# Kernel optimization log

Measured on AMD Instinct MI355X. Metric: run time of the kernel, lower is better.

The kernel has to match this reference:

```python
import jax, jax.numpy as jnp
import numpy as np

EPS = 1e-8

def setup_inputs() -> dict:
    key = jax.random.key(0)
    k1, k2 = jax.random.split(key)
    B, N, M, D = 8, 4096, 4096, 3
    x1 = jax.random.normal(k1, (B, N, D), dtype=jnp.float32)
    y1 = jax.random.normal(k2, (B, M, D), dtype=jnp.float32)
    return {"x1": x1, "y1": y1}

def reference(x1, y1):
    # Faithful to: dist = sqrt(1e-8 + sum((x1[:,None,:,:] - y1[:,:,None,:])**2, -1))
    # computed via the Gram-matrix expansion to avoid the (B,M,N,D) intermediate.
    x_sq = jnp.sum(x1 * x1, axis=-1)                 # (B, N)
    y_sq = jnp.sum(y1 * y1, axis=-1)                 # (B, M)
    xy = jnp.einsum('bmd,bnd->bmn', y1, x1)          # (B, M, N)
    d2 = jnp.maximum(y_sq[:, :, None] + x_sq[:, None, :] - 2.0 * xy, 0.0)
    dist = jnp.sqrt(EPS + d2)                        # (B, M, N)
    min1 = jnp.min(dist, axis=1)                     # (B, N): nearest y for each x
    min2 = jnp.min(dist, axis=2)                     # (B, M): nearest x for each y
    return jnp.mean(min1) + jnp.mean(min2)
```

## Files before the change

### kernel.cpp

```cpp
#include <hip/hip_runtime.h>

constexpr int B = 8;
constexpr int N = 4096;
constexpr int PTS = B * N;
constexpr int TOT = 2 * PTS;

#define TPB 256
#define R 4
#define CHUNK 128
#define NCHUNK (N / CHUNK)
#define NTILE (N / (TPB * R))

__global__ __launch_bounds__(256) void prep(
        const float* __restrict__ x1, const float* __restrict__ y1,
        float4* __restrict__ qpre, float* __restrict__ out) {
    int tid = blockIdx.x * 256 + threadIdx.x;
    if (tid == 0) out[0] = 0.0f;
    if (tid >= TOT) return;
    int dir = tid >> 15;
    int p   = tid & (PTS - 1);
    const float* src = dir ? x1 : y1;
    float qx = src[3 * p], qy = src[3 * p + 1], qz = src[3 * p + 2];
    float qq = fmaf(qx, qx, fmaf(qy, qy, qz * qz));
    qpre[tid] = make_float4(qx, qy, qz, qq);
}

__global__ __launch_bounds__(TPB) void chamfer_min3(
        const float* __restrict__ x1, const float* __restrict__ y1,
        const float4* __restrict__ qpre,
        float* __restrict__ partials) {
    __shared__ float4 qs[CHUNK];

    const int dir   = blockIdx.y / NCHUNK;
    const int chunk = blockIdx.y % NCHUNK;
    const int b     = blockIdx.z;
    const int tile  = blockIdx.x;

    const float4* qp = qpre + (size_t)dir * PTS + (size_t)b * N + chunk * CHUNK;
    if (threadIdx.x < CHUNK) qs[threadIdx.x] = qp[threadIdx.x];

    const float* own = dir ? y1 : x1;
    const int ibase = tile * (TPB * R) + threadIdx.x;
    float mx[R], my[R], mz[R], xx[R], acc[R];
    #pragma unroll
    for (int r = 0; r < R; r++) {
        const float* pp = own + ((size_t)b * N + ibase + r * TPB) * 3;
        float px = pp[0], py = pp[1], pz = pp[2];
        mx[r] = -2.0f * px; my[r] = -2.0f * py; mz[r] = -2.0f * pz;
        xx[r] = fmaf(px, px, fmaf(py, py, pz * pz));
        acc[r] = 3.4e38f;
    }

    __syncthreads();

    #pragma unroll 4
    for (int j = 0; j < CHUNK; j++) {
        float4 q = qs[j];
        #pragma unroll
        for (int r = 0; r < R; r++) {
            float g = fmaf(mx[r], q.x, fmaf(my[r], q.y, fmaf(mz[r], q.z, q.w)));
            acc[r] = fminf(acc[r], g);
        }
    }

    float* dst = partials + (size_t)chunk * TOT + (size_t)dir * PTS + (size_t)b * N;
    #pragma unroll
    for (int r = 0; r < R; r++) {
        dst[ibase + r * TPB] = fmaxf(acc[r] + xx[r], 0.0f);
    }
}

__global__ __launch_bounds__(256) void chamfer_finish(
        const float* __restrict__ partials, float* __restrict__ out, float scale) {
    int p = blockIdx.x * 256 + threadIdx.x;
    float m = partials[p];
    #pragma unroll
    for (int c = 1; c < NCHUNK; c++) m = fminf(m, partials[(size_t)c * TOT + p]);
    float s = sqrtf(1e-8f + m) * scale;

    #pragma unroll
    for (int off = 32; off > 0; off >>= 1) s += __shfl_down(s, off, 64);

    __shared__ float partial[4];
    const int wid = threadIdx.x >> 6, lane = threadIdx.x & 63;
    if (lane == 0) partial[wid] = s;
    __syncthreads();
    if (threadIdx.x == 0) {
        atomicAdd(out, partial[0] + partial[1] + partial[2] + partial[3]);
    }
}

extern "C" void kernel_launch(void* const* d_in, const int* in_sizes, int n_in,
                              void* d_out, int out_size, void* d_ws, size_t ws_size,
                              hipStream_t stream) {
    const float* x1 = (const float*)d_in[0];
    const float* y1 = (const float*)d_in[1];
    float* out = (float*)d_out;

    float4* qpre    = (float4*)d_ws;
    float* partials = (float*)(qpre + TOT);

    prep<<<TOT / 256, 256, 0, stream>>>(x1, y1, qpre, out);

    dim3 grid(NTILE, 2 * NCHUNK, B);
    chamfer_min3<<<grid, TPB, 0, stream>>>(x1, y1, qpre, partials);

    chamfer_finish<<<TOT / 256, 256, 0, stream>>>(partials, out, 1.0f / (B * N));
}
```

Measured before the change: 84.69 us.

## Fuse prep into main kernel and use packed FP32 FMA with more rows per thread

Removes the separate prep kernel: each block now builds its shared query chunk directly from the raw inputs and zeroes the output itself. The inner loop is rewritten with inline v_pk_fma_f32 assembly so one instruction evaluates the distance expansion for two owned points. Rows per thread double from 4 to 8, which halves the number of tiles. The aim is to cut VALU issue count and one launch, at the cost of more registers per thread and fewer blocks in the grid.

```diff
diff --git a/kernel.cpp b/kernel.cpp
--- a/kernel.cpp
+++ b/kernel.cpp
@@ -6,67 +6,82 @@
 constexpr int TOT = 2 * PTS;
 
 #define TPB 256
-#define R 4
+#define R 8
+#define RP (R / 2)
 #define CHUNK 128
-#define NCHUNK (N / CHUNK)
+#define KC (N / CHUNK)
 #define NTILE (N / (TPB * R))
 
-__global__ __launch_bounds__(256) void prep(
+typedef float float2v __attribute__((ext_vector_type(2)));
+
+__global__ __launch_bounds__(TPB) void chamfer_min4(
         const float* __restrict__ x1, const float* __restrict__ y1,
-        float4* __restrict__ qpre, float* __restrict__ out) {
-    int tid = blockIdx.x * 256 + threadIdx.x;
-    if (tid == 0) out[0] = 0.0f;
-    if (tid >= TOT) return;
-    int dir = tid >> 15;
-    int p   = tid & (PTS - 1);
-    const float* src = dir ? x1 : y1;
-    float qx = src[3 * p], qy = src[3 * p + 1], qz = src[3 * p + 2];
-    float qq = fmaf(qx, qx, fmaf(qy, qy, qz * qz));
-    qpre[tid] = make_float4(qx, qy, qz, qq);
-}
-
-__global__ __launch_bounds__(TPB) void chamfer_min3(
-        const float* __restrict__ x1, const float* __restrict__ y1,
-        const float4* __restrict__ qpre,
-        float* __restrict__ partials) {
+        float* __restrict__ partials,
+        float* __restrict__ out) {
     __shared__ float4 qs[CHUNK];
 
-    const int dir   = blockIdx.y / NCHUNK;
-    const int chunk = blockIdx.y % NCHUNK;
+    if (blockIdx.x == 0 && blockIdx.y == 0 && blockIdx.z == 0 && threadIdx.x == 0)
+        out[0] = 0.0f;
+
+    const int dir   = blockIdx.y / KC;
+    const int chunk = blockIdx.y % KC;
     const int b     = blockIdx.z;
     const int tile  = blockIdx.x;
 
-    const float4* qp = qpre + (size_t)dir * PTS + (size_t)b * N + chunk * CHUNK;
-    if (threadIdx.x < CHUNK) qs[threadIdx.x] = qp[threadIdx.x];
+    const float* own = dir ? y1 : x1;
+    const float* oth = dir ? x1 : y1;
 
-    const float* own = dir ? y1 : x1;
+    if (threadIdx.x < CHUNK) {
+        const float* op = oth + ((size_t)b * N + chunk * CHUNK + threadIdx.x) * 3;
+        float qx = op[0], qy = op[1], qz = op[2];
+        qs[threadIdx.x] = make_float4(qx, qy, qz, fmaf(qx, qx, fmaf(qy, qy, qz * qz)));
+    }
+
     const int ibase = tile * (TPB * R) + threadIdx.x;
-    float mx[R], my[R], mz[R], xx[R], acc[R];
+    float2v mx2[RP], my2[RP], mz2[RP], acc2[RP];
+    float xx[R];
     #pragma unroll
-    for (int r = 0; r < R; r++) {
-        const float* pp = own + ((size_t)b * N + ibase + r * TPB) * 3;
-        float px = pp[0], py = pp[1], pz = pp[2];
-        mx[r] = -2.0f * px; my[r] = -2.0f * py; mz[r] = -2.0f * pz;
-        xx[r] = fmaf(px, px, fmaf(py, py, pz * pz));
-        acc[r] = 3.4e38f;
+    for (int p = 0; p < RP; p++) {
+        #pragma unroll
+        for (int e = 0; e < 2; e++) {
+            const int r = 2 * p + e;
+            const float* pp = own + ((size_t)b * N + ibase + r * TPB) * 3;
+            float px = pp[0], py = pp[1], pz = pp[2];
+            mx2[p][e] = -2.0f * px;
+            my2[p][e] = -2.0f * py;
+            mz2[p][e] = -2.0f * pz;
+            xx[r] = fmaf(px, px, fmaf(py, py, pz * pz));
+        }
+        acc2[p] = float2v{3.4e38f, 3.4e38f};
     }
 
     __syncthreads();
 
-    #pragma unroll 4
+    #pragma unroll 2
     for (int j = 0; j < CHUNK; j++) {
-        float4 q = qs[j];
+        union { float4 f4; float2v f2[2]; } qa;
+        qa.f4 = qs[j];
+        float2v xy = qa.f2[0];
+        float2v zw = qa.f2[1];
         #pragma unroll
-        for (int r = 0; r < R; r++) {
-            float g = fmaf(mx[r], q.x, fmaf(my[r], q.y, fmaf(mz[r], q.z, q.w)));
-            acc[r] = fminf(acc[r], g);
+        for (int p = 0; p < RP; p++) {
+            float2v g;
+            asm("v_pk_fma_f32 %0, %1, %2, %1 op_sel:[0,0,1] op_sel_hi:[0,1,1]"
+                : "=v"(g) : "v"(zw), "v"(mz2[p]));
+            asm("v_pk_fma_f32 %0, %1, %2, %3 op_sel:[1,0,0] op_sel_hi:[1,1,1]"
+                : "=v"(g) : "v"(xy), "v"(my2[p]), "v"(g));
+            asm("v_pk_fma_f32 %0, %1, %2, %3 op_sel:[0,0,0] op_sel_hi:[0,1,1]"
+                : "=v"(g) : "v"(xy), "v"(mx2[p]), "v"(g));
+            acc2[p].x = fminf(acc2[p].x, g.x);
+            acc2[p].y = fminf(acc2[p].y, g.y);
         }
     }
 
     float* dst = partials + (size_t)chunk * TOT + (size_t)dir * PTS + (size_t)b * N;
     #pragma unroll
-    for (int r = 0; r < R; r++) {
-        dst[ibase + r * TPB] = fmaxf(acc[r] + xx[r], 0.0f);
+    for (int p = 0; p < RP; p++) {
+        dst[ibase + (2 * p) * TPB]     = fmaxf(acc2[p].x + xx[2 * p], 0.0f);
+        dst[ibase + (2 * p + 1) * TPB] = fmaxf(acc2[p].y + xx[2 * p + 1], 0.0f);
     }
 }
 
@@ -75,7 +90,7 @@
     int p = blockIdx.x * 256 + threadIdx.x;
     float m = partials[p];
     #pragma unroll
-    for (int c = 1; c < NCHUNK; c++) m = fminf(m, partials[(size_t)c * TOT + p]);
+    for (int c = 1; c < KC; c++) m = fminf(m, partials[(size_t)c * TOT + p]);
     float s = sqrtf(1e-8f + m) * scale;
 
     #pragma unroll
@@ -97,13 +112,10 @@
     const float* y1 = (const float*)d_in[1];
     float* out = (float*)d_out;
 
-    float4* qpre    = (float4*)d_ws;
-    float* partials = (float*)(qpre + TOT);
+    float* partials = (float*)d_ws;
 
-    prep<<<TOT / 256, 256, 0, stream>>>(x1, y1, qpre, out);
-
-    dim3 grid(NTILE, 2 * NCHUNK, B);
-    chamfer_min3<<<grid, TPB, 0, stream>>>(x1, y1, qpre, partials);
+    dim3 grid(NTILE, 2 * KC, B);
+    chamfer_min4<<<grid, TPB, 0, stream>>>(x1, y1, partials, out);
 
     chamfer_finish<<<TOT / 256, 256, 0, stream>>>(partials, out, 1.0f / (B * N));
 }
```

After: 82.75 us. 1.02x faster.
